# Performance work log

Measured on AMD Instinct MI355X. Metric: run time of the kernel, lower is better.

Reference implementation:

```python
import jax, jax.numpy as jnp
import numpy as np

B, H, W, C = 16, 64, 64, 256
NH = 8
KD = C // NH  # 32
SCALE = KD ** -0.5


def rotate_every_two(x):
    x1 = x[..., ::2]
    x2 = x[..., 1::2]
    return jnp.stack([-x2, x1], axis=-1).reshape(x.shape)


def theta_shift(x, sin, cos):
    return x * cos + rotate_every_two(x) * sin


def dwconv2d(x, w, b):
    # x: (b,h,w,c), w: (5,5,1,c) HWIO depthwise, pad 2
    y = jax.lax.conv_general_dilated(
        x, w, window_strides=(1, 1), padding=((2, 2), (2, 2)),
        dimension_numbers=("NHWC", "HWIO", "NHWC"), feature_group_count=x.shape[-1])
    return y + b


def setup_inputs() -> dict:
    key = jax.random.key(0)
    ks = jax.random.split(key, 12)
    s = 0.02
    return {
        "x": jax.random.normal(ks[0], (B, H, W, C), jnp.float32),
        "sin": jax.random.uniform(ks[1], (H, W, KD), jnp.float32, -1.0, 1.0),
        "cos": jax.random.uniform(ks[2], (H, W, KD), jnp.float32, -1.0, 1.0),
        "mask_h": jax.random.normal(ks[3], (NH, H, H), jnp.float32) * 0.1,
        "mask_w": jax.random.normal(ks[4], (NH, W, W), jnp.float32) * 0.1,
        "Wq": jax.random.normal(ks[5], (C, C), jnp.float32) * s,
        "bq": jnp.zeros((C,), jnp.float32),
        "Wk": jax.random.normal(ks[6], (C, C), jnp.float32) * s,
        "bk": jnp.zeros((C,), jnp.float32),
        "Wv": jax.random.normal(ks[7], (C, C), jnp.float32) * s,
        "bv": jnp.zeros((C,), jnp.float32),
        "conv_w": jax.random.normal(ks[8], (5, 5, 1, C), jnp.float32) * s,
        "conv_b": jnp.zeros((C,), jnp.float32),
        "Wo": jax.random.normal(ks[9], (C, C), jnp.float32) * s,
        "bo": jnp.zeros((C,), jnp.float32),
    }


def reference(x, sin, cos, mask_h, mask_w, Wq, bq, Wk, bk, Wv, bv, conv_w, conv_b, Wo, bo):
    b, h, w, _ = x.shape
    n = mask_w.shape[0]
    kd = sin.shape[-1]

    q = x @ Wq + bq
    k = (x @ Wk + bk) * SCALE
    v = x @ Wv + bv
    lepe = dwconv2d(v, conv_w, conv_b)

    # (b,n,h,w,d)
    q = q.reshape(b, h, w, n, kd).transpose(0, 3, 1, 2, 4)
    k = k.reshape(b, h, w, n, kd).transpose(0, 3, 1, 2, 4)
    qr = theta_shift(q, sin, cos)
    kr = theta_shift(k, sin, cos)

    # width attention: rows independent
    qk_w = jnp.einsum("bhnwd,bhnvd->bhnwv", qr.transpose(0, 2, 1, 3, 4), kr.transpose(0, 2, 1, 3, 4))
    qk_w = jax.nn.softmax(qk_w + mask_w, axis=-1)
    vv = v.reshape(b, h, w, n, -1).transpose(0, 1, 3, 2, 4)  # (b,h,n,w,d2)
    vv = jnp.einsum("bhnwv,bhnvd->bhnwd", qk_w, vv)

    # height attention: columns independent
    qr_h = qr.transpose(0, 3, 1, 2, 4)  # (b,w,n,h,d)
    kr_h = kr.transpose(0, 3, 1, 2, 4)
    vv = vv.transpose(0, 3, 2, 1, 4)  # (b,w,n,h,d2)
    qk_h = jnp.einsum("bwnhd,bwngd->bwnhg", qr_h, kr_h)
    qk_h = jax.nn.softmax(qk_h + mask_h, axis=-1)
    out = jnp.einsum("bwnhg,bwngd->bwnhd", qk_h, vv)

    out = out.transpose(0, 3, 1, 2, 4).reshape(b, h, w, -1)  # (b,h,w,n*d2)
    out = out + lepe
    return out @ Wo + bo
```

## Files before the change

kernel.cpp:

```cpp
#include <hip/hip_runtime.h>

typedef __attribute__((ext_vector_type(8))) short bf16x8;
typedef __attribute__((ext_vector_type(4))) float f32x4;

constexpr int B  = 16;
constexpr int H  = 64;
constexpr int W  = 64;
constexpr int C  = 256;
constexpr int NH = 8;
constexpr int KD = 32;
constexpr float SCALE = 0.17677669529663687f;
constexpr int M_TOT = B * H * W;
constexpr size_t NEL = (size_t)B * H * W * C;

__device__ __forceinline__ unsigned short f2bf(float f) {
    union { float f; unsigned int u; } x; x.f = f;
    unsigned int u = x.u;
    unsigned int r = (u + 0x7fffu + ((u >> 16) & 1u)) >> 16;
    return (unsigned short)r;
}
__device__ __forceinline__ float bf2f(unsigned short s) {
    union { unsigned int u; float f; } x; x.u = ((unsigned int)s) << 16; return x.f;
}
__device__ __forceinline__ float bf_lo(unsigned int u) {
    union { unsigned int u; float f; } x; x.u = u << 16; return x.f;
}
__device__ __forceinline__ float bf_hi(unsigned int u) {
    union { unsigned int u; float f; } x; x.u = u & 0xffff0000u; return x.f;
}
__device__ __forceinline__ unsigned int pack2(float a, float b) {
    return (unsigned int)f2bf(a) | ((unsigned int)f2bf(b) << 16);
}
__device__ __forceinline__ void cvt8(uint4 rv, float* f) {
    f[0] = bf_lo(rv.x); f[1] = bf_hi(rv.x); f[2] = bf_lo(rv.y); f[3] = bf_hi(rv.y);
    f[4] = bf_lo(rv.z); f[5] = bf_hi(rv.z); f[6] = bf_lo(rv.w); f[7] = bf_hi(rv.w);
}
__device__ __forceinline__ int swz(int row, int kp8) {
    return row * 32 + (kp8 ^ (((row >> 2) & 3) << 3));
}

__global__ __launch_bounds__(256) void prep_all(
    const float* __restrict__ x, unsigned short* __restrict__ x16,
    const float* __restrict__ Wq, const float* __restrict__ Wk,
    const float* __restrict__ Wv, const float* __restrict__ Wo,
    unsigned short* __restrict__ wdst)
{
    int bid = blockIdx.x;
    if (bid < 8192) {
        size_t i8 = ((size_t)bid * 256 + threadIdx.x) * 8;
        float4 f0 = *(const float4*)(x + i8);
        float4 f1 = *(const float4*)(x + i8 + 4);
        uint4 o;
        o.x = pack2(f0.x, f0.y); o.y = pack2(f0.z, f0.w);
        o.z = pack2(f1.x, f1.y); o.w = pack2(f1.z, f1.w);
        *(uint4*)(x16 + i8) = o;
    } else {
        int tidg = (bid - 8192) * 256 + threadIdx.x;
        int mat = tidg >> 13;
        int lt  = tidg & 8191;
        int n = lt >> 5, k0 = (lt & 31) << 3;
        const float* __restrict__ src = (mat == 0) ? Wq : (mat == 1) ? Wk : (mat == 2) ? Wv : Wo;
        unsigned int p[4];
#pragma unroll
        for (int j = 0; j < 4; ++j) {
            float a  = src[(size_t)(k0 + 2 * j) * 256 + n];
            float b2 = src[(size_t)(k0 + 2 * j + 1) * 256 + n];
            p[j] = pack2(a, b2);
        }
        uint4 o = {p[0], p[1], p[2], p[3]};
        *(uint4*)(wdst + ((size_t)mat * 65536) + (size_t)n * 256 + k0) = o;
    }
}

__global__ __launch_bounds__(256) void qkv_mfma(
    const unsigned short* __restrict__ x16, const unsigned short* __restrict__ Wt16,
    const float* __restrict__ bq, const float* __restrict__ bk, const float* __restrict__ bv,
    const float* __restrict__ sin_t, const float* __restrict__ cos_t,
    unsigned short* __restrict__ qr, unsigned short* __restrict__ kr,
    unsigned short* __restrict__ v16)
{
    __shared__ __align__(16) unsigned short As[128 * 32];
    __shared__ __align__(16) unsigned short Bs[128 * 32];

    const int t = threadIdx.x;
    const int lane = t & 63, wid = t >> 6;
    const int wr = wid >> 1, wc = wid & 1;
    const int m0 = blockIdx.x * 128;
    const int n0 = blockIdx.y * 128;
    const int matid = blockIdx.y >> 1;
    const int nb = n0 & 255;

    f32x4 acc[4][4];
#pragma unroll
    for (int i = 0; i < 4; ++i)
#pragma unroll
        for (int j = 0; j < 4; ++j)
#pragma unroll
            for (int q = 0; q < 4; ++q) acc[i][j][q] = 0.f;

    const int row_s = t >> 2;
    const int kp_s  = (t & 3) << 3;

    for (int ks = 0; ks < 8; ++ks) {
        const int k0 = ks * 32;
        const unsigned short* ap = x16 + (size_t)(m0 + row_s) * 256 + k0 + kp_s;
        uint4 a0 = *(const uint4*)ap;
        uint4 a1 = *(const uint4*)(ap + 64 * 256);
        const unsigned short* bp = Wt16 + (size_t)(n0 + row_s) * 256 + k0 + kp_s;
        uint4 b0 = *(const uint4*)bp;
        uint4 b1 = *(const uint4*)(bp + 64 * 256);

        __syncthreads();
        *(uint4*)(&As[swz(row_s,      kp_s)]) = a0;
        *(uint4*)(&As[swz(row_s + 64, kp_s)]) = a1;
        *(uint4*)(&Bs[swz(row_s,      kp_s)]) = b0;
        *(uint4*)(&Bs[swz(row_s + 64, kp_s)]) = b1;
        __syncthreads();

        bf16x8 af[4], bf[4];
        const int rsel = lane & 15, kg8 = (lane >> 4) << 3;
#pragma unroll
        for (int i = 0; i < 4; ++i)
            af[i] = *(const bf16x8*)(&As[swz(wr * 64 + i * 16 + rsel, kg8)]);
#pragma unroll
        for (int j = 0; j < 4; ++j)
            bf[j] = *(const bf16x8*)(&Bs[swz(wc * 64 + j * 16 + rsel, kg8)]);
#pragma unroll
        for (int i = 0; i < 4; ++i)
#pragma unroll
            for (int j = 0; j < 4; ++j)
                acc[i][j] = __builtin_amdgcn_mfma_f32_16x16x32_bf16(bf[j], af[i], acc[i][j], 0, 0, 0);
    }

    const int col_l = lane & 15, rowg = (lane >> 4) << 2;
    if (matid == 2) {
#pragma unroll
        for (int i = 0; i < 4; ++i) {
            const int m = m0 + wr * 64 + i * 16 + col_l;
#pragma unroll
            for (int j = 0; j < 4; ++j) {
                const int nn = nb + wc * 64 + j * 16 + rowg;
                float4 bias4 = *(const float4*)(bv + nn);
                ushort4 o;
                o.x = f2bf(acc[i][j][0] + bias4.x);
                o.y = f2bf(acc[i][j][1] + bias4.y);
                o.z = f2bf(acc[i][j][2] + bias4.z);
                o.w = f2bf(acc[i][j][3] + bias4.w);
                *(ushort4*)(v16 + (size_t)m * 256 + nn) = o;
            }
        }
    } else {
        const float sc = matid ? SCALE : 1.0f;
        const float* __restrict__ bias = matid ? bk : bq;
        unsigned short* __restrict__ dst = matid ? kr : qr;
#pragma unroll
        for (int i = 0; i < 4; ++i) {
            const int m = m0 + wr * 64 + i * 16 + col_l;
            const int bb = m >> 12, hh = (m >> 6) & 63, ww = m & 63;
            const size_t pixbase = ((size_t)hh * 64 + ww) * 32;
#pragma unroll
            for (int j = 0; j < 4; ++j) {
                const int n = nb + wc * 64 + j * 16 + rowg;
                const int nh = n >> 5, db = n & 31;
                float4 bias4 = *(const float4*)(bias + n);
                float4 cs4 = *(const float4*)(cos_t + pixbase + db);
                float4 sn4 = *(const float4*)(sin_t + pixbase + db);
                float v0 = (acc[i][j][0] + bias4.x) * sc;
                float v1 = (acc[i][j][1] + bias4.y) * sc;
                float v2 = (acc[i][j][2] + bias4.z) * sc;
                float v3 = (acc[i][j][3] + bias4.w) * sc;
                ushort4 o;
                o.x = f2bf(v0 * cs4.x - v1 * sn4.x);
                o.y = f2bf(v1 * cs4.y + v0 * sn4.y);
                o.z = f2bf(v2 * cs4.z - v3 * sn4.z);
                o.w = f2bf(v3 * cs4.w + v2 * sn4.w);
                *(ushort4*)(dst + ((((size_t)bb * 8 + nh) * 64 + hh) * 64 + ww) * 32 + db) = o;
            }
        }
    }
}

__global__ __launch_bounds__(256) void conv_kernel(
    const unsigned short* __restrict__ v, const float* __restrict__ cw,
    const float* __restrict__ cb, unsigned short* __restrict__ lepe)
{
    size_t tid = (size_t)blockIdx.x * 256 + threadIdx.x;
    const int c8 = (int)(tid & 31) << 3;
    const int w0 = ((int)(tid >> 5) & 15) << 2;
    const int h  = (int)(tid >> 9) & 63;
    const int b  = (int)(tid >> 15);

    float acc[4][8];
    {
        float4 cb0 = *(const float4*)(cb + c8);
        float4 cb1 = *(const float4*)(cb + c8 + 4);
#pragma unroll
        for (int o = 0; o < 4; ++o) {
            acc[o][0] = cb0.x; acc[o][1] = cb0.y; acc[o][2] = cb0.z; acc[o][3] = cb0.w;
            acc[o][4] = cb1.x; acc[o][5] = cb1.y; acc[o][6] = cb1.z; acc[o][7] = cb1.w;
        }
    }

    const unsigned short* __restrict__ vb = v + (size_t)b * 4096 * 256 + c8;
#pragma unroll
    for (int dy = 0; dy < 5; ++dy) {
        const int yy = h + dy - 2;
        if (yy < 0 || yy >= 64) continue;
        float rowf[8][8];
#pragma unroll
        for (int j = 0; j < 8; ++j) {
            const int xx = w0 + j - 2;
            if (xx < 0 || xx >= 64) {
#pragma unroll
                for (int q = 0; q < 8; ++q) rowf[j][q] = 0.f;
            } else {
                uint4 rv = *(const uint4*)(vb + (size_t)(yy * 64 + xx) * 256);
                cvt8(rv, rowf[j]);
            }
        }
#pragma unroll
        for (int dx = 0; dx < 5; ++dx) {
            const float* wp = cw + (dy * 5 + dx) * 256 + c8;
            float4 wv0 = *(const float4*)wp;
            float4 wv1 = *(const float4*)(wp + 4);
#pragma unroll
            for (int o = 0; o < 4; ++o) {
                const float* rf = rowf[dx + o];
                acc[o][0] += rf[0] * wv0.x; acc[o][1] += rf[1] * wv0.y;
                acc[o][2] += rf[2] * wv0.z; acc[o][3] += rf[3] * wv0.w;
                acc[o][4] += rf[4] * wv1.x; acc[o][5] += rf[5] * wv1.y;
                acc[o][6] += rf[6] * wv1.z; acc[o][7] += rf[7] * wv1.w;
            }
        }
    }

    unsigned short* __restrict__ op = lepe + (((size_t)(b * 64 + h) * 64) + w0) * 256 + c8;
#pragma unroll
    for (int o = 0; o < 4; ++o) {
        uint4 ov;
        ov.x = pack2(acc[o][0], acc[o][1]); ov.y = pack2(acc[o][2], acc[o][3]);
        ov.z = pack2(acc[o][4], acc[o][5]); ov.w = pack2(acc[o][6], acc[o][7]);
        *(uint4*)(op + (size_t)o * 256) = ov;
    }
}

template <int AXIS>
__global__ __launch_bounds__(256) void attn_mfma(
    const unsigned short* __restrict__ qr, const unsigned short* __restrict__ kr,
    const unsigned short* __restrict__ vin, const float* __restrict__ mask,
    const unsigned short* __restrict__ addin, unsigned short* __restrict__ outp)
{
    __shared__ __align__(16) short qs[64 * 40];
    __shared__ __align__(16) short ks[64 * 40];
    __shared__ __align__(16) short vt[32 * 72];
    __shared__ __align__(16) short P [64 * 72];

    const int t    = threadIdx.x;
    const int lane = t & 63, wv = t >> 6;
    const int bid  = blockIdx.x;
    const int nh   = bid & 7;
    const int pos  = (bid >> 3) & 63;
    const int b    = bid >> 9;

    size_t qbase, vbase;
    int qstride, vstride;
    if (AXIS == 0) {
        qbase   = ((size_t)(b * 8 + nh) * 64 + pos) * 2048;
        qstride = 32;
        vbase   = ((size_t)(b * 64 + pos) * 64) * 256 + nh * 32;
        vstride = 256;
    } else {
        qbase   = ((size_t)(b * 8 + nh) * 64) * 2048 + pos * 32;
        qstride = 2048;
        vbase   = ((size_t)b * 64 * 64) * 256 + pos * 256 + nh * 32;
        vstride = 16384;
    }

    {
        int row = t >> 2, c8 = (t & 3) << 3;
        uint4 rq = *(const uint4*)(qr + qbase + (size_t)row * qstride + c8);
        *(uint4*)(&qs[row * 40 + c8]) = rq;
        uint4 rk = *(const uint4*)(kr + qbase + (size_t)row * qstride + c8);
        *(uint4*)(&ks[row * 40 + c8]) = rk;
        uint4 rv = *(const uint4*)(vin + vbase + (size_t)row * vstride + c8);
        const unsigned short* pv = (const unsigned short*)&rv;
#pragma unroll
        for (int j = 0; j < 8; ++j) vt[(c8 + j) * 72 + row] = pv[j];
    }
    __syncthreads();

    const int rsel = lane & 15;
    const int kg   = (lane >> 4) << 3;
    const int rowg = (lane >> 4) << 2;

    bf16x8 aq = *(const bf16x8*)(&qs[(wv * 16 + rsel) * 40 + kg]);
    f32x4 s[4];
#pragma unroll
    for (int j = 0; j < 4; ++j) {
        f32x4 z = {0.f, 0.f, 0.f, 0.f};
        bf16x8 bk8 = *(const bf16x8*)(&ks[(j * 16 + rsel) * 40 + kg]);
        s[j] = __builtin_amdgcn_mfma_f32_16x16x32_bf16(aq, bk8, z, 0, 0, 0);
    }

    const float* __restrict__ mrow = mask + (size_t)nh * 4096;
#pragma unroll
    for (int r = 0; r < 4; ++r) {
        const int grow = wv * 16 + rowg + r;
#pragma unroll
        for (int j = 0; j < 4; ++j)
            s[j][r] += mrow[grow * 64 + j * 16 + rsel];
        float mx = fmaxf(fmaxf(s[0][r], s[1][r]), fmaxf(s[2][r], s[3][r]));
        mx = fmaxf(mx, __shfl_xor(mx, 1));
        mx = fmaxf(mx, __shfl_xor(mx, 2));
        mx = fmaxf(mx, __shfl_xor(mx, 4));
        mx = fmaxf(mx, __shfl_xor(mx, 8));
        float e0 = __expf(s[0][r] - mx), e1 = __expf(s[1][r] - mx);
        float e2 = __expf(s[2][r] - mx), e3 = __expf(s[3][r] - mx);
        float sum = e0 + e1 + e2 + e3;
        sum += __shfl_xor(sum, 1);
        sum += __shfl_xor(sum, 2);
        sum += __shfl_xor(sum, 4);
        sum += __shfl_xor(sum, 8);
        float inv = 1.0f / sum;
        P[grow * 72 +      rsel] = f2bf(e0 * inv);
        P[grow * 72 + 16 + rsel] = f2bf(e1 * inv);
        P[grow * 72 + 32 + rsel] = f2bf(e2 * inv);
        P[grow * 72 + 48 + rsel] = f2bf(e3 * inv);
    }
    __syncthreads();

    f32x4 o[2];
#pragma unroll
    for (int n = 0; n < 2; ++n)
#pragma unroll
        for (int q = 0; q < 4; ++q) o[n][q] = 0.f;
#pragma unroll
    for (int kk = 0; kk < 2; ++kk) {
        bf16x8 ap = *(const bf16x8*)(&P[(wv * 16 + rsel) * 72 + kk * 32 + kg]);
#pragma unroll
        for (int n = 0; n < 2; ++n) {
            bf16x8 bv8 = *(const bf16x8*)(&vt[(n * 16 + rsel) * 72 + kk * 32 + kg]);
            o[n] = __builtin_amdgcn_mfma_f32_16x16x32_bf16(ap, bv8, o[n], 0, 0, 0);
        }
    }

#pragma unroll
    for (int n = 0; n < 2; ++n)
#pragma unroll
        for (int r = 0; r < 4; ++r) {
            const int grow = wv * 16 + rowg + r;
            size_t oidx = vbase + (size_t)grow * vstride + n * 16 + rsel;
            float val = o[n][r];
            if (AXIS == 1) val += bf2f(addin[oidx]);
            outp[oidx] = f2bf(val);
        }
}

__global__ __launch_bounds__(256) void gemm_out_mfma(
    const unsigned short* __restrict__ y16, const unsigned short* __restrict__ Wot16,
    const float* __restrict__ bo, float* __restrict__ out)
{
    __shared__ __align__(16) unsigned short As[128 * 32];
    __shared__ __align__(16) unsigned short Bs[128 * 32];

    const int t = threadIdx.x;
    const int lane = t & 63, wid = t >> 6;
    const int wr = wid >> 1, wc = wid & 1;
    const int m0 = blockIdx.x * 128;
    const int n0 = blockIdx.y * 128;

    f32x4 acc[4][4];
#pragma unroll
    for (int i = 0; i < 4; ++i)
#pragma unroll
        for (int j = 0; j < 4; ++j)
#pragma unroll
            for (int q = 0; q < 4; ++q) acc[i][j][q] = 0.f;

    const int row_s = t >> 2;
    const int kp_s  = (t & 3) << 3;

    for (int ks = 0; ks < 8; ++ks) {
        const int k0 = ks * 32;
        const unsigned short* ap = y16 + (size_t)(m0 + row_s) * 256 + k0 + kp_s;
        uint4 a0 = *(const uint4*)ap;
        uint4 a1 = *(const uint4*)(ap + 64 * 256);
        const unsigned short* bp = Wot16 + (size_t)(n0 + row_s) * 256 + k0 + kp_s;
        uint4 b0 = *(const uint4*)bp;
        uint4 b1 = *(const uint4*)(bp + 64 * 256);

        __syncthreads();
        *(uint4*)(&As[swz(row_s,      kp_s)]) = a0;
        *(uint4*)(&As[swz(row_s + 64, kp_s)]) = a1;
        *(uint4*)(&Bs[swz(row_s,      kp_s)]) = b0;
        *(uint4*)(&Bs[swz(row_s + 64, kp_s)]) = b1;
        __syncthreads();

        bf16x8 af[4], bf[4];
        const int rsel = lane & 15, kg8 = (lane >> 4) << 3;
#pragma unroll
        for (int i = 0; i < 4; ++i)
            af[i] = *(const bf16x8*)(&As[swz(wr * 64 + i * 16 + rsel, kg8)]);
#pragma unroll
        for (int j = 0; j < 4; ++j)
            bf[j] = *(const bf16x8*)(&Bs[swz(wc * 64 + j * 16 + rsel, kg8)]);
#pragma unroll
        for (int i = 0; i < 4; ++i)
#pragma unroll
            for (int j = 0; j < 4; ++j)
                acc[i][j] = __builtin_amdgcn_mfma_f32_16x16x32_bf16(af[i], bf[j], acc[i][j], 0, 0, 0);
    }

    const int col_l = lane & 15, rowg = (lane >> 4) << 2;
#pragma unroll
    for (int i = 0; i < 4; ++i)
#pragma unroll
        for (int j = 0; j < 4; ++j) {
            int nn = n0 + wc * 64 + j * 16 + col_l;
            float bias = bo[nn];
#pragma unroll
            for (int r = 0; r < 4; ++r) {
                int m = m0 + wr * 64 + i * 16 + rowg + r;
                out[(size_t)m * 256 + nn] = acc[i][j][r] + bias;
            }
        }
}

extern "C" void kernel_launch(void* const* d_in, const int* in_sizes, int n_in,
                              void* d_out, int out_size, void* d_ws, size_t ws_size,
                              hipStream_t stream) {
    const float* x      = (const float*)d_in[0];
    const float* sin_t  = (const float*)d_in[1];
    const float* cos_t  = (const float*)d_in[2];
    const float* mask_h = (const float*)d_in[3];
    const float* mask_w = (const float*)d_in[4];
    const float* Wq     = (const float*)d_in[5];
    const float* bq     = (const float*)d_in[6];
    const float* Wk     = (const float*)d_in[7];
    const float* bk     = (const float*)d_in[8];
    const float* Wv     = (const float*)d_in[9];
    const float* bv     = (const float*)d_in[10];
    const float* conv_w = (const float*)d_in[11];
    const float* conv_b = (const float*)d_in[12];
    const float* Wo     = (const float*)d_in[13];
    const float* bo     = (const float*)d_in[14];

    unsigned short* ws    = (unsigned short*)d_ws;
    unsigned short* v16   = ws;
    unsigned short* lepe16= v16 + NEL;
    unsigned short* qr16  = lepe16 + NEL;
    unsigned short* kr16  = qr16 + NEL;
    unsigned short* y16   = kr16 + NEL;
    unsigned short* Wt16  = y16 + NEL;
    unsigned short* Wot16 = Wt16 + 768 * 256;

    unsigned short* vv16 = (unsigned short*)d_out;
    unsigned short* x16  = (unsigned short*)d_out + NEL;

    prep_all<<<8192 + 128, 256, 0, stream>>>(x, x16, Wq, Wk, Wv, Wo, Wt16);

    qkv_mfma<<<dim3(M_TOT / 128, 6), 256, 0, stream>>>(
        x16, Wt16, bq, bk, bv, sin_t, cos_t, qr16, kr16, v16);

    conv_kernel<<<(int)(NEL / 32 / 256), 256, 0, stream>>>(v16, conv_w, conv_b, lepe16);

    attn_mfma<0><<<B * H * NH, 256, 0, stream>>>(qr16, kr16, v16, mask_w, nullptr, vv16);

    attn_mfma<1><<<B * W * NH, 256, 0, stream>>>(qr16, kr16, vv16, mask_h, lepe16, y16);

    gemm_out_mfma<<<dim3(M_TOT / 128, 2), 256, 0, stream>>>(y16, Wot16, bo, (float*)d_out);
}
```

Measured before the change: 240.9 us.

## Pre-swizzle QKV weights into MFMA fragment layout and load B operand directly

The prep kernel now writes the Q/K/V weights in a per-lane MFMA fragment order. The QKV GEMM then reads each B fragment straight from global memory as one 16-byte load instead of staging it through shared memory. This removes the B tile's shared-memory stores and reads and halves LDS use in the QKV GEMM. The cost is more global and L2 traffic per k-step, since each wave fetches its own fragments with no reuse across waves.

```diff
diff --git a/kernel.cpp b/kernel.cpp
--- a/kernel.cpp
+++ b/kernel.cpp
@@ -58,37 +58,54 @@
         int tidg = (bid - 8192) * 256 + threadIdx.x;
         int mat = tidg >> 13;
         int lt  = tidg & 8191;
-        int n = lt >> 5, k0 = (lt & 31) << 3;
         const float* __restrict__ src = (mat == 0) ? Wq : (mat == 1) ? Wk : (mat == 2) ? Wv : Wo;
-        unsigned int p[4];
-#pragma unroll
-        for (int j = 0; j < 4; ++j) {
-            float a  = src[(size_t)(k0 + 2 * j) * 256 + n];
-            float b2 = src[(size_t)(k0 + 2 * j + 1) * 256 + n];
-            p[j] = pack2(a, b2);
-        }
-        uint4 o = {p[0], p[1], p[2], p[3]};
-        *(uint4*)(wdst + ((size_t)mat * 65536) + (size_t)n * 256 + k0) = o;
+        if (mat < 3) {
+            int lane = lt & 63;
+            int ks   = (lt >> 6) & 7;
+            int g    = lt >> 9;
+            int n    = g * 16 + (lane & 15);
+            int k0   = ks * 32 + ((lane >> 4) << 3);
+            unsigned int p[4];
+#pragma unroll
+            for (int j = 0; j < 4; ++j) {
+                float a  = src[(size_t)(k0 + 2 * j) * 256 + n];
+                float b2 = src[(size_t)(k0 + 2 * j + 1) * 256 + n];
+                p[j] = pack2(a, b2);
+            }
+            uint4 o = {p[0], p[1], p[2], p[3]};
+            *(uint4*)(wdst + ((size_t)mat * 65536) + (size_t)lt * 8) = o;
+        } else {
+            int n = lt >> 5, k0 = (lt & 31) << 3;
+            unsigned int p[4];
+#pragma unroll
+            for (int j = 0; j < 4; ++j) {
+                float a  = src[(size_t)(k0 + 2 * j) * 256 + n];
+                float b2 = src[(size_t)(k0 + 2 * j + 1) * 256 + n];
+                p[j] = pack2(a, b2);
+            }
+            uint4 o = {p[0], p[1], p[2], p[3]};
+            *(uint4*)(wdst + ((size_t)3 * 65536) + (size_t)n * 256 + k0) = o;
+        }
     }
 }
 
 __global__ __launch_bounds__(256) void qkv_mfma(
-    const unsigned short* __restrict__ x16, const unsigned short* __restrict__ Wt16,
+    const unsigned short* __restrict__ x16, const unsigned short* __restrict__ wf,
     const float* __restrict__ bq, const float* __restrict__ bk, const float* __restrict__ bv,
     const float* __restrict__ sin_t, const float* __restrict__ cos_t,
     unsigned short* __restrict__ qr, unsigned short* __restrict__ kr,
     unsigned short* __restrict__ v16)
 {
     __shared__ __align__(16) unsigned short As[128 * 32];
-    __shared__ __align__(16) unsigned short Bs[128 * 32];
 
     const int t = threadIdx.x;
     const int lane = t & 63, wid = t >> 6;
     const int wr = wid >> 1, wc = wid & 1;
     const int m0 = blockIdx.x * 128;
-    const int n0 = blockIdx.y * 128;
-    const int matid = blockIdx.y >> 1;
-    const int nb = n0 & 255;
+    const int yb = blockIdx.y;
+    const int matid = yb >> 1;
+    const int nb = (yb & 1) * 128;
+    const int gb = yb * 8 + wc * 4;
 
     f32x4 acc[4][4];
 #pragma unroll
@@ -106,15 +123,10 @@
         const unsigned short* ap = x16 + (size_t)(m0 + row_s) * 256 + k0 + kp_s;
         uint4 a0 = *(const uint4*)ap;
         uint4 a1 = *(const uint4*)(ap + 64 * 256);
-        const unsigned short* bp = Wt16 + (size_t)(n0 + row_s) * 256 + k0 + kp_s;
-        uint4 b0 = *(const uint4*)bp;
-        uint4 b1 = *(const uint4*)(bp + 64 * 256);
 
         __syncthreads();
         *(uint4*)(&As[swz(row_s,      kp_s)]) = a0;
         *(uint4*)(&As[swz(row_s + 64, kp_s)]) = a1;
-        *(uint4*)(&Bs[swz(row_s,      kp_s)]) = b0;
-        *(uint4*)(&Bs[swz(row_s + 64, kp_s)]) = b1;
         __syncthreads();
 
         bf16x8 af[4], bf[4];
@@ -124,7 +136,7 @@
             af[i] = *(const bf16x8*)(&As[swz(wr * 64 + i * 16 + rsel, kg8)]);
 #pragma unroll
         for (int j = 0; j < 4; ++j)
-            bf[j] = *(const bf16x8*)(&Bs[swz(wc * 64 + j * 16 + rsel, kg8)]);
+            bf[j] = *(const bf16x8*)(wf + (((size_t)(gb + j) * 8 + ks) * 64 + lane) * 8);
 #pragma unroll
         for (int i = 0; i < 4; ++i)
 #pragma unroll
@@ -134,12 +146,13 @@
 
     const int col_l = lane & 15, rowg = (lane >> 4) << 2;
     if (matid == 2) {
+        const int nbv = (yb - 4) * 128;
 #pragma unroll
         for (int i = 0; i < 4; ++i) {
             const int m = m0 + wr * 64 + i * 16 + col_l;
 #pragma unroll
             for (int j = 0; j < 4; ++j) {
-                const int nn = nb + wc * 64 + j * 16 + rowg;
+                const int nn = nbv + wc * 64 + j * 16 + rowg;
                 float4 bias4 = *(const float4*)(bv + nn);
                 ushort4 o;
                 o.x = f2bf(acc[i][j][0] + bias4.x);
@@ -451,16 +464,16 @@
     unsigned short* qr16  = lepe16 + NEL;
     unsigned short* kr16  = qr16 + NEL;
     unsigned short* y16   = kr16 + NEL;
-    unsigned short* Wt16  = y16 + NEL;
-    unsigned short* Wot16 = Wt16 + 768 * 256;
+    unsigned short* wf    = y16 + NEL;
+    unsigned short* Wot16 = wf + 3 * 65536;
 
     unsigned short* vv16 = (unsigned short*)d_out;
     unsigned short* x16  = (unsigned short*)d_out + NEL;
 
-    prep_all<<<8192 + 128, 256, 0, stream>>>(x, x16, Wq, Wk, Wv, Wo, Wt16);
+    prep_all<<<8192 + 128, 256, 0, stream>>>(x, x16, Wq, Wk, Wv, Wo, wf);
 
     qkv_mfma<<<dim3(M_TOT / 128, 6), 256, 0, stream>>>(
-        x16, Wt16, bq, bk, bv, sin_t, cos_t, qr16, kr16, v16);
+        x16, wf, bq, bk, bv, sin_t, cos_t, qr16, kr16, v16);
 
     conv_kernel<<<(int)(NEL / 32 / 256), 256, 0, stream>>>(v16, conv_w, conv_b, lepe16);
 
```

Result: slower. 250.3 us (+3.9%).
